# Kernel tuning notes

Measured on AMD Instinct MI355X. Metric: run time of the kernel, lower is better.

The kernel has to match this reference:

```python
import jax, jax.numpy as jnp
import numpy as np

LAMBDA_SMOOTH = 0.1

def setup_inputs() -> dict:
    key = jax.random.key(0)
    adj = jax.random.normal(key, (8192, 8192), dtype=jnp.float32)
    return {"adj": adj}

def reference(adj) -> jnp.ndarray:
    # 5-point Laplacian smoothness over interior pixels i,j in [1, N-1)
    center = adj[1:-1, 1:-1]
    neigh_avg = (adj[:-2, 1:-1] + adj[2:, 1:-1] + adj[1:-1, :-2] + adj[1:-1, 2:]) * 0.25
    smoothness = jnp.sum(jnp.abs(center - neigh_avg))
    return LAMBDA_SMOOTH * smoothness
```

## Files before the change

kernel.cpp:

```cpp
#include <hip/hip_runtime.h>


#define N 8192
#define ROWS_PER_BLOCK 64
#define TPB 256
#define COL_BLOCKS (N / (4 * TPB))
#define ROW_BLOCKS ((N - 2 + ROWS_PER_BLOCK - 1) / ROWS_PER_BLOCK)
#define NUM_PARTIALS (COL_BLOCKS * ROW_BLOCKS)

__global__ __launch_bounds__(TPB) void smooth_partial(const float* __restrict__ a,
                                                      float* __restrict__ partial) {
    const int tid  = threadIdx.x;
    const int lane = tid & 63;
    const int c0   = (blockIdx.x * TPB + tid) * 4;
    const int r0   = 1 + blockIdx.y * ROWS_PER_BLOCK;
    const int r1   = min(r0 + ROWS_PER_BLOCK - 1, N - 2);

    float4 p = *(const float4*)(a + (size_t)(r0 - 1) * N + c0);
    float4 c = *(const float4*)(a + (size_t)r0 * N + c0);

    float acc = 0.0f;

    for (int r = r0; r <= r1; ++r) {
        float4 n = *(const float4*)(a + (size_t)(r + 1) * N + c0);

        float left  = __shfl_up(c.w, 1);
        float right = __shfl_down(c.x, 1);
        if (lane == 0)  left  = (c0 > 0)      ? a[(size_t)r * N + c0 - 1] : 0.0f;
        if (lane == 63) right = (c0 + 4 < N)  ? a[(size_t)r * N + c0 + 4] : 0.0f;

        if (c0 >= 1) {
            float d = c.x - 0.25f * (p.x + n.x + left + c.y);
            acc += fabsf(d);
        }
        {
            float d = c.y - 0.25f * (p.y + n.y + c.x + c.z);
            acc += fabsf(d);
        }
        {
            float d = c.z - 0.25f * (p.z + n.z + c.y + c.w);
            acc += fabsf(d);
        }
        if (c0 + 3 <= N - 2) {
            float d = c.w - 0.25f * (p.w + n.w + c.z + right);
            acc += fabsf(d);
        }

        p = c;
        c = n;
    }

    for (int off = 32; off; off >>= 1) acc += __shfl_down(acc, off);

    __shared__ float wsum[TPB / 64];
    if (lane == 0) wsum[tid >> 6] = acc;
    __syncthreads();
    if (tid == 0) {
        float s = 0.0f;
        #pragma unroll
        for (int w = 0; w < TPB / 64; ++w) s += wsum[w];
        partial[blockIdx.y * gridDim.x + blockIdx.x] = s;
    }
}

__global__ __launch_bounds__(256) void reduce_final(const float* __restrict__ partial,
                                                    int n, float* __restrict__ out) {
    __shared__ double sh[256];
    double s = 0.0;
    for (int i = threadIdx.x; i < n; i += 256) s += (double)partial[i];
    sh[threadIdx.x] = s;
    __syncthreads();
    for (int stride = 128; stride; stride >>= 1) {
        if (threadIdx.x < stride) sh[threadIdx.x] += sh[threadIdx.x + stride];
        __syncthreads();
    }
    if (threadIdx.x == 0) out[0] = (float)(0.1 * sh[0]);
}

extern "C" void kernel_launch(void* const* d_in, const int* in_sizes, int n_in,
                              void* d_out, int out_size, void* d_ws, size_t ws_size,
                              hipStream_t stream) {
    const float* a   = (const float*)d_in[0];
    float* out       = (float*)d_out;
    float* partial   = (float*)d_ws;

    dim3 grid(COL_BLOCKS, ROW_BLOCKS);
    smooth_partial<<<grid, TPB, 0, stream>>>(a, partial);
    reduce_final<<<1, 256, 0, stream>>>(partial, NUM_PARTIALS, out);
}
```

Before: 48.65 us.

## Fuse final reduction via atomicAdd, unroll row loop by two, double rows per block

```diff
diff --git a/kernel.cpp b/kernel.cpp
--- a/kernel.cpp
+++ b/kernel.cpp
@@ -2,52 +2,56 @@
 
 
 #define N 8192
-#define ROWS_PER_BLOCK 64
+#define ROWS_PER_BLOCK 128
 #define TPB 256
 #define COL_BLOCKS (N / (4 * TPB))
 #define ROW_BLOCKS ((N - 2 + ROWS_PER_BLOCK - 1) / ROWS_PER_BLOCK)
-#define NUM_PARTIALS (COL_BLOCKS * ROW_BLOCKS)
 
-__global__ __launch_bounds__(TPB) void smooth_partial(const float* __restrict__ a,
-                                                      float* __restrict__ partial) {
+__global__ __launch_bounds__(TPB) void smooth_fused(const float* __restrict__ a,
+                                                    float* __restrict__ out) {
     const int tid  = threadIdx.x;
     const int lane = tid & 63;
     const int c0   = (blockIdx.x * TPB + tid) * 4;
     const int r0   = 1 + blockIdx.y * ROWS_PER_BLOCK;
     const int r1   = min(r0 + ROWS_PER_BLOCK - 1, N - 2);
 
-    float4 p = *(const float4*)(a + (size_t)(r0 - 1) * N + c0);
-    float4 c = *(const float4*)(a + (size_t)r0 * N + c0);
+    const float* base = a + c0;
+    float4 p = *(const float4*)(base + (size_t)(r0 - 1) * N);
+    float4 c = *(const float4*)(base + (size_t)r0 * N);
 
     float acc = 0.0f;
 
-    for (int r = r0; r <= r1; ++r) {
-        float4 n = *(const float4*)(a + (size_t)(r + 1) * N + c0);
+    for (int r = r0; r <= r1; r += 2) {
+        float4 n1 = *(const float4*)(base + (size_t)(r + 1) * N);
+        float4 n2 = *(const float4*)(base + (size_t)(r + 2) * N);
 
-        float left  = __shfl_up(c.w, 1);
-        float right = __shfl_down(c.x, 1);
-        if (lane == 0)  left  = (c0 > 0)      ? a[(size_t)r * N + c0 - 1] : 0.0f;
-        if (lane == 63) right = (c0 + 4 < N)  ? a[(size_t)r * N + c0 + 4] : 0.0f;
-
-        if (c0 >= 1) {
-            float d = c.x - 0.25f * (p.x + n.x + left + c.y);
-            acc += fabsf(d);
+        {
+            float left  = __shfl_up(c.w, 1);
+            float right = __shfl_down(c.x, 1);
+            if (lane == 0  && c0 > 0)     left  = a[(size_t)r * N + c0 - 1];
+            if (lane == 63 && c0 + 4 < N) right = a[(size_t)r * N + c0 + 4];
+            if (c0 >= 1)
+                acc += fabsf(c.x - 0.25f * (p.x + n1.x + left + c.y));
+            acc += fabsf(c.y - 0.25f * (p.y + n1.y + c.x + c.z));
+            acc += fabsf(c.z - 0.25f * (p.z + n1.z + c.y + c.w));
+            if (c0 + 3 <= N - 2)
+                acc += fabsf(c.w - 0.25f * (p.w + n1.w + c.z + right));
         }
         {
-            float d = c.y - 0.25f * (p.y + n.y + c.x + c.z);
-            acc += fabsf(d);
-        }
-        {
-            float d = c.z - 0.25f * (p.z + n.z + c.y + c.w);
-            acc += fabsf(d);
-        }
-        if (c0 + 3 <= N - 2) {
-            float d = c.w - 0.25f * (p.w + n.w + c.z + right);
-            acc += fabsf(d);
+            float left  = __shfl_up(n1.w, 1);
+            float right = __shfl_down(n1.x, 1);
+            if (lane == 0  && c0 > 0)     left  = a[(size_t)(r + 1) * N + c0 - 1];
+            if (lane == 63 && c0 + 4 < N) right = a[(size_t)(r + 1) * N + c0 + 4];
+            if (c0 >= 1)
+                acc += fabsf(n1.x - 0.25f * (c.x + n2.x + left + n1.y));
+            acc += fabsf(n1.y - 0.25f * (c.y + n2.y + n1.x + n1.z));
+            acc += fabsf(n1.z - 0.25f * (c.z + n2.z + n1.y + n1.w));
+            if (c0 + 3 <= N - 2)
+                acc += fabsf(n1.w - 0.25f * (c.w + n2.w + n1.z + right));
         }
 
-        p = c;
-        c = n;
+        p = n1;
+        c = n2;
     }
 
     for (int off = 32; off; off >>= 1) acc += __shfl_down(acc, off);
@@ -59,32 +63,18 @@
         float s = 0.0f;
         #pragma unroll
         for (int w = 0; w < TPB / 64; ++w) s += wsum[w];
-        partial[blockIdx.y * gridDim.x + blockIdx.x] = s;
+        atomicAdd(out, 0.1f * s);
     }
-}
-
-__global__ __launch_bounds__(256) void reduce_final(const float* __restrict__ partial,
-                                                    int n, float* __restrict__ out) {
-    __shared__ double sh[256];
-    double s = 0.0;
-    for (int i = threadIdx.x; i < n; i += 256) s += (double)partial[i];
-    sh[threadIdx.x] = s;
-    __syncthreads();
-    for (int stride = 128; stride; stride >>= 1) {
-        if (threadIdx.x < stride) sh[threadIdx.x] += sh[threadIdx.x + stride];
-        __syncthreads();
-    }
-    if (threadIdx.x == 0) out[0] = (float)(0.1 * sh[0]);
 }
 
 extern "C" void kernel_launch(void* const* d_in, const int* in_sizes, int n_in,
                               void* d_out, int out_size, void* d_ws, size_t ws_size,
                               hipStream_t stream) {
-    const float* a   = (const float*)d_in[0];
-    float* out       = (float*)d_out;
-    float* partial   = (float*)d_ws;
+    const float* a = (const float*)d_in[0];
+    float* out     = (float*)d_out;
+
+    hipMemsetAsync(out, 0, sizeof(float), stream);
 
     dim3 grid(COL_BLOCKS, ROW_BLOCKS);
-    smooth_partial<<<grid, TPB, 0, stream>>>(a, partial);
-    reduce_final<<<1, 256, 0, stream>>>(partial, NUM_PARTIALS, out);
+    smooth_fused<<<grid, TPB, 0, stream>>>(a, out);
 }
```

After: 67.57 us. 38.9% more time.
